# Kernel tuning notes

Hardware: AMD Instinct MI355X
Metric: run time of the kernel (lower is better)

Reference implementation:

```python
import jax, jax.numpy as jnp
import numpy as np

DISCOUNT = 0.997
LAMBDA = 0.95
LOSS_SCALE = 0.5
NUM_BINS = 255
BIN_LO, BIN_HI = -20.0, 20.0


def setup_inputs() -> dict:
    key = jax.random.key(0)
    k0, k1, k2, k3 = jax.random.split(key, 4)
    B, H, D = 1024, 16, 4096
    latents = jax.random.normal(k0, (B, H, D), dtype=jnp.float32)
    rewards = jax.random.normal(k1, (B, H), dtype=jnp.float32)
    dones = jnp.zeros((B, H), dtype=jnp.float32)
    bootstrap_latent = jax.random.normal(k2, (B, D), dtype=jnp.float32)
    W = jax.random.normal(k3, (D, NUM_BINS), dtype=jnp.float32) * (1.0 / np.sqrt(D))
    b = jnp.zeros((NUM_BINS,), dtype=jnp.float32)
    return {"latents": latents, "rewards": rewards, "dones": dones,
            "bootstrap_latent": bootstrap_latent, "W": W, "b": b}


def _bin_centers():
    return jnp.linspace(BIN_LO, BIN_HI, NUM_BINS, dtype=jnp.float32)


def _value_head(x, W, b):
    # x: (N, D) -> logits (N, K), value (N,)
    logits = x @ W + b
    value = jax.nn.softmax(logits, axis=-1) @ _bin_centers()
    return value, logits


def _target_to_bins(returns_flat):
    # two-hot encoding onto uniform bins; returns (N, K) soft target
    step = (BIN_HI - BIN_LO) / (NUM_BINS - 1)
    pos = (jnp.clip(returns_flat, BIN_LO, BIN_HI) - BIN_LO) / step  # in [0, K-1]
    low = jnp.clip(jnp.floor(pos).astype(jnp.int32), 0, NUM_BINS - 2)
    frac = pos - low.astype(pos.dtype)
    oh_lo = jax.nn.one_hot(low, NUM_BINS, dtype=returns_flat.dtype)
    oh_hi = jax.nn.one_hot(low + 1, NUM_BINS, dtype=returns_flat.dtype)
    return (1.0 - frac)[:, None] * oh_lo + frac[:, None] * oh_hi


def _lambda_returns(rewards, values, dones, bootstrap_value):
    # backward linear recurrence: G_t = r_t + gamma*mask_t*((1-lam)*V_{t+1} + lam*G_{t+1})
    next_values = jnp.concatenate([values[:, 1:], bootstrap_value[:, None]], axis=1)
    xs = (rewards.T, next_values.T, (1.0 - dones).T)  # time-major (H, B)

    def step(carry, x):
        r, nv, m = x
        g = r + DISCOUNT * m * ((1.0 - LAMBDA) * nv + LAMBDA * carry)
        return g, g

    _, outs = jax.lax.scan(step, bootstrap_value, xs, reverse=True)
    return outs.T  # (B, H)


def reference(latents, rewards, dones, bootstrap_latent, W, b):
    B, H = rewards.shape
    flat_latents = latents.reshape(-1, latents.shape[-1])  # (B*H, D)
    values_flat, logits = _value_head(flat_latents, W, b)
    values = values_flat.reshape(B, H)

    bootstrap_value, _ = _value_head(bootstrap_latent, W, b)
    bootstrap_value = jax.lax.stop_gradient(bootstrap_value)

    returns = jax.lax.stop_gradient(
        _lambda_returns(rewards, jax.lax.stop_gradient(values), dones, bootstrap_value))

    target = _target_to_bins(returns.reshape(-1))  # (B*H, K)
    logp = jax.nn.log_softmax(logits, axis=-1)
    value_loss = jnp.mean(-jnp.sum(target * logp, axis=-1))
    total_loss = LOSS_SCALE * value_loss

    return jnp.stack([total_loss, value_loss, values.mean(), returns.mean(),
                      jnp.std(values, ddof=1), jnp.std(returns, ddof=1)])
```

## Files before the change

### kernel.cpp

```cpp
#include <hip/hip_runtime.h>
#include <math.h>

#define NBINS 255
#define BIN_LO_F (-20.0f)
#define BIN_HI_F (20.0f)

typedef __attribute__((ext_vector_type(8))) short short8;
typedef __attribute__((ext_vector_type(16))) float f32x16;

__device__ __forceinline__ unsigned short f2bf(float f) {
    unsigned u = __builtin_bit_cast(unsigned, f);
    unsigned r = u + 0x7fffu + ((u >> 16) & 1u);
    return (unsigned short)(r >> 16);
}

__device__ __forceinline__ unsigned pkbf(float lo, float hi) {
    unsigned d;
    asm("v_cvt_pk_bf16_f32 %0, %1, %2" : "=v"(d) : "v"(lo), "v"(hi));
    return d;
}

__device__ __forceinline__ short8 mk8(unsigned a, unsigned b, unsigned c, unsigned d) {
    union { unsigned u[4]; short8 s; } t;
    t.u[0] = a; t.u[1] = b; t.u[2] = c; t.u[3] = d;
    return t.s;
}

__device__ __forceinline__ void glds16(const void* g, void* l) {
    __builtin_amdgcn_global_load_lds(
        (const __attribute__((address_space(1))) unsigned int*)g,
        (__attribute__((address_space(3))) unsigned int*)l, 16, 0, 0);
}

__device__ __forceinline__ double wave_reduce_sum_d(double v) {
    #pragma unroll
    for (int m = 32; m >= 1; m >>= 1) v += __shfl_xor(v, m, 64);
    return v;
}

__global__ __launch_bounds__(256) void pack_w5(
    const float* __restrict__ W, char* __restrict__ WpackB)
{
    int u = blockIdx.x * 256 + threadIdx.x;
    int kt = u >> 9;
    int v  = u & 511;
    int lh = v >> 8;
    int gcol = (v >> 5) & 7;
    int c31  = v & 31;
    int col  = gcol * 32 + c31;
    int k0   = kt * 16 + lh * 8;
    short8 s;
    #pragma unroll
    for (int e = 0; e < 8; ++e)
        s[e] = (col < NBINS) ? (short)f2bf(W[(size_t)(k0 + e) * NBINS + col]) : (short)0;
    *(short8*)(WpackB + (size_t)u * 16) = s;
}

__global__ __launch_bounds__(256, 4) void gemm_mfma_v10(
    const float* __restrict__ latents, const float* __restrict__ boot,
    const char* __restrict__ WpackB, float* __restrict__ P0, float* __restrict__ P1,
    int NR, int R, int D, int nMt)
{
    __shared__ __align__(16) char ldsA[2][4096];
    __shared__ __align__(16) char ldsB[2][8192];

    const int tid  = threadIdx.x;
    const int wave = tid >> 6, lane = tid & 63;
    const int l31  = lane & 31, lhi = lane >> 5;
    const int mw   = wave & 1, nw = wave >> 1;
    const int KH   = D >> 1;
    const int NT   = KH >> 4;

    int bid  = blockIdx.x;
    int work = (bid & 7) * 68 + (bid >> 3);
    const int kh = (work >= nMt) ? 1 : 0;
    const int mt = work - kh * nMt;
    const int row0 = mt * 64;
    float* __restrict__ P = kh ? P1 : P0;

    int arow = row0 + lane; if (arow > R - 1) arow = R - 1;
    const float* arowp = (arow < NR) ? latents + (size_t)arow * D
                                     : boot + (size_t)(arow - NR) * D;
    const float* asrc = arowp + kh * KH + wave * 4;
    const char*  bbase = WpackB + (size_t)kh * ((size_t)NT * 8192)
                                + (wave << 11) + (lane << 4);

    f32x16 acc[4];
    #pragma unroll
    for (int g = 0; g < 4; ++g)
        #pragma unroll
        for (int r = 0; r < 16; ++r) acc[g][r] = 0.f;

#define STAGE(T, BUF) do {                                                  \
        glds16(asrc + (size_t)(T) * 16, &ldsA[BUF][(wave << 10) + (lane << 4)]); \
        const char* bs_ = bbase + (size_t)(T) * 8192;                       \
        char* bd_ = &ldsB[BUF][(wave << 11) + (lane << 4)];                 \
        glds16(bs_,        bd_);                                            \
        glds16(bs_ + 1024, bd_ + 1024);                                     \
    } while (0)

#define COMPUTE(BUF) do {                                                   \
        const char* ab_ = &ldsA[BUF][0] + (lhi << 11) + (mw << 9) + (l31 << 4); \
        const char* bb_ = &ldsB[BUF][0] + (lhi << 12) + (nw << 11) + (l31 << 4); \
        float4 f0_ = *(const float4*)(ab_);                                 \
        float4 f1_ = *(const float4*)(ab_ + 1024);                          \
        short8 a_ = mk8(pkbf(f0_.x, f0_.y), pkbf(f0_.z, f0_.w),             \
                        pkbf(f1_.x, f1_.y), pkbf(f1_.z, f1_.w));            \
        _Pragma("unroll")                                                   \
        for (int g = 0; g < 4; ++g) {                                       \
            short8 b_ = *(const short8*)(bb_ + (g << 9));                   \
            acc[g] = __builtin_amdgcn_mfma_f32_32x32x16_bf16(a_, b_, acc[g], 0, 0, 0); \
        }                                                                   \
    } while (0)

#define BAR()   __builtin_amdgcn_s_barrier()
#define SCHED() __builtin_amdgcn_sched_barrier(0)
#define WAITV3() asm volatile("s_waitcnt vmcnt(3)" ::: "memory")
#define WAITV0() asm volatile("s_waitcnt vmcnt(0)" ::: "memory")

    STAGE(0, 0);

    int t = 0;
    for (; t + 3 < NT; t += 2) {
        BAR(); SCHED(); STAGE(t + 1, 1); SCHED(); WAITV3(); BAR(); SCHED(); COMPUTE(0);
        BAR(); SCHED(); STAGE(t + 2, 0); SCHED(); WAITV3(); BAR(); SCHED(); COMPUTE(1);
    }
    BAR(); SCHED(); STAGE(NT - 1, 1); SCHED(); WAITV3(); BAR(); SCHED(); COMPUTE(0);
    BAR(); SCHED(); WAITV0(); BAR(); SCHED(); COMPUTE(1);

#undef STAGE
#undef COMPUTE
#undef BAR
#undef SCHED
#undef WAITV3
#undef WAITV0

    #pragma unroll
    for (int g = 0; g < 4; ++g) {
        int col = nw * 128 + g * 32 + l31;
        #pragma unroll
        for (int r = 0; r < 16; ++r) {
            int row = row0 + mw * 32 + (r & 3) + 8 * (r >> 2) + 4 * lhi;
            P[(size_t)row * 256 + col] = acc[g][r];
        }
    }
}

__global__ __launch_bounds__(256) void softmax_stats2(
    const float* __restrict__ P0, const float* __restrict__ P1,
    const float* __restrict__ bvec, float* __restrict__ values,
    float* __restrict__ logZ, int R)
{
    int row  = blockIdx.x * 4 + (threadIdx.x >> 6);
    int lane = threadIdx.x & 63;
    if (row >= R) return;
    const float* p0 = P0 + (size_t)row * 256;
    const float* p1 = P1 + (size_t)row * 256;
    const float step = (float)(40.0 / 254.0);

    float l[4];
    float m = -INFINITY;
    #pragma unroll
    for (int u = 0; u < 4; ++u) {
        int idx = lane + 64 * u;
        l[u] = (idx < NBINS) ? (p0[idx] + p1[idx] + bvec[idx]) : -INFINITY;
        m = fmaxf(m, l[u]);
    }
    #pragma unroll
    for (int sh = 32; sh >= 1; sh >>= 1) m = fmaxf(m, __shfl_xor(m, sh, 64));

    float s = 0.f, sc = 0.f;
    #pragma unroll
    for (int u = 0; u < 4; ++u) {
        int idx = lane + 64 * u;
        if (idx < NBINS) {
            float e = __expf(l[u] - m);
            s  += e;
            sc += e * (BIN_LO_F + step * (float)idx);
        }
    }
    #pragma unroll
    for (int sh = 32; sh >= 1; sh >>= 1) {
        s  += __shfl_xor(s, sh, 64);
        sc += __shfl_xor(sc, sh, 64);
    }
    if (lane == 0) {
        values[row] = sc / s;
        logZ[row]   = m + __logf(s);
    }
}

__global__ void lambda_returns_k(
    const float* __restrict__ rewards, const float* __restrict__ dones,
    const float* __restrict__ values, float* __restrict__ returns,
    int B, int H, int NR)
{
    int b = blockIdx.x * blockDim.x + threadIdx.x;
    if (b >= B) return;
    const float gamma = 0.997f;
    const float lam   = 0.95f;
    const float oml   = (float)(1.0 - 0.95);
    float bootv = values[NR + b];
    float g = bootv;
    for (int h = H - 1; h >= 0; --h) {
        float nv   = (h == H - 1) ? bootv : values[b * H + h + 1];
        float mask = 1.0f - dones[b * H + h];
        g = rewards[b * H + h] + gamma * mask * (oml * nv + lam * g);
        returns[b * H + h] = g;
    }
}

__global__ __launch_bounds__(256) void loss_moments2(
    const float* __restrict__ P0, const float* __restrict__ P1,
    const float* __restrict__ bvec, const float* __restrict__ logZ,
    const float* __restrict__ values, const float* __restrict__ returns,
    double* __restrict__ accum, int NR)
{
    int row = blockIdx.x * blockDim.x + threadIdx.x;
    double lsum = 0, vsum = 0, v2 = 0, rsum = 0, r2 = 0;
    if (row < NR) {
        float v   = values[row];
        float ret = returns[row];
        float cl  = fminf(fmaxf(ret, BIN_LO_F), BIN_HI_F);
        const float step = (float)(40.0 / 254.0);
        float pos = (cl - BIN_LO_F) / step;
        int low = (int)floorf(pos);
        low = min(max(low, 0), NBINS - 2);
        float frac = pos - (float)low;
        size_t base = (size_t)row * 256;
        float llo = P0[base + low]     + P1[base + low]     + bvec[low];
        float lhi = P0[base + low + 1] + P1[base + low + 1] + bvec[low + 1];
        float loss = logZ[row] - (1.f - frac) * llo - frac * lhi;
        lsum = (double)loss;
        vsum = (double)v;   v2 = (double)v * (double)v;
        rsum = (double)ret; r2 = (double)ret * (double)ret;
    }
    lsum = wave_reduce_sum_d(lsum);
    vsum = wave_reduce_sum_d(vsum);
    v2   = wave_reduce_sum_d(v2);
    rsum = wave_reduce_sum_d(rsum);
    r2   = wave_reduce_sum_d(r2);
    if ((threadIdx.x & 63) == 0) {
        atomicAdd(&accum[0], lsum);
        atomicAdd(&accum[1], vsum);
        atomicAdd(&accum[2], v2);
        atomicAdd(&accum[3], rsum);
        atomicAdd(&accum[4], r2);
    }
}

__global__ void finalize_k(const double* __restrict__ accum,
                           float* __restrict__ out, int NR)
{
    if (threadIdx.x == 0 && blockIdx.x == 0) {
        double n  = (double)NR;
        double vl = accum[0] / n;
        double mv = accum[1] / n;
        double vv = (accum[2] - n * mv * mv) / (n - 1.0);
        double mr = accum[3] / n;
        double vr = (accum[4] - n * mr * mr) / (n - 1.0);
        out[0] = (float)(0.5 * vl);
        out[1] = (float)vl;
        out[2] = (float)mv;
        out[3] = (float)mr;
        out[4] = (float)sqrt(vv > 0.0 ? vv : 0.0);
        out[5] = (float)sqrt(vr > 0.0 ? vr : 0.0);
    }
}

extern "C" void kernel_launch(void* const* d_in, const int* in_sizes, int n_in,
                              void* d_out, int out_size, void* d_ws, size_t ws_size,
                              hipStream_t stream) {
    const float* latents = (const float*)d_in[0];
    const float* rewards = (const float*)d_in[1];
    const float* dones   = (const float*)d_in[2];
    const float* boot    = (const float*)d_in[3];
    const float* W       = (const float*)d_in[4];
    const float* bvec    = (const float*)d_in[5];
    float* out = (float*)d_out;

    const int BH = in_sizes[1];
    const int D  = in_sizes[0] / BH;
    const int B  = in_sizes[3] / D;
    const int H  = BH / B;
    const int NR = BH;
    const int R  = NR + B;

    char* ws = (char*)d_ws;
    size_t off = 0;
    float* P0 = (float*)(ws + off); off += (size_t)R * 256 * sizeof(float);
    float* P1 = (float*)(ws + off); off += (size_t)R * 256 * sizeof(float);
    float* values = (float*)(ws + off); off += (size_t)R * sizeof(float);
    float* logZ   = (float*)(ws + off); off += (size_t)R * sizeof(float);
    float* rets   = (float*)(ws + off); off += (size_t)NR * sizeof(float);
    off = (off + 255) & ~(size_t)255;
    double* accum = (double*)(ws + off); off += 64;
    off = (off + 255) & ~(size_t)255;
    char* WpackB  = ws + off; off += (size_t)(D / 16) * 8192;

    hipMemsetAsync(accum, 0, 64, stream);

    const int packUnits = (D / 16) * 512;
    pack_w5<<<packUnits / 256, 256, 0, stream>>>(W, WpackB);

    const int nMt = R / 64;
    const int nwg = nMt * 2;
    gemm_mfma_v10<<<nwg, 256, 0, stream>>>(latents, boot, WpackB, P0, P1,
                                           NR, R, D, nMt);
    softmax_stats2<<<(R + 3) / 4, 256, 0, stream>>>(P0, P1, bvec, values, logZ, R);
    lambda_returns_k<<<(B + 255) / 256, 256, 0, stream>>>(rewards, dones, values, rets, B, H, NR);
    loss_moments2<<<(NR + 255) / 256, 256, 0, stream>>>(P0, P1, bvec, logZ, values, rets, accum, NR);
    finalize_k<<<1, 64, 0, stream>>>(accum, out, NR);
}
```

Before: 191.0 us.

## Generalize split-K to four partials and swizzle A-tile LDS layout

Generalizes the GEMM's K split from a fixed two halves to a runtime split (four when the workspace is large enough), so the grid launches twice as many workgroups over R/64 row tiles. It also changes how A rows are loaded into LDS, with an XOR swizzle on 16-byte chunks, to cut bank conflicts on the float4 reads. The softmax and loss kernels now sum the split partials in a loop. In exchange it writes and rereads twice as many partial logit buffers, which adds memory traffic, and it depends on ws_size being large enough.

```diff
diff --git a/kernel.cpp b/kernel.cpp
--- a/kernel.cpp
+++ b/kernel.cpp
@@ -56,10 +56,10 @@
     *(short8*)(WpackB + (size_t)u * 16) = s;
 }
 
-__global__ __launch_bounds__(256, 4) void gemm_mfma_v10(
+__global__ __launch_bounds__(256, 4) void gemm_mfma_v11(
     const float* __restrict__ latents, const float* __restrict__ boot,
-    const char* __restrict__ WpackB, float* __restrict__ P0, float* __restrict__ P1,
-    int NR, int R, int D, int nMt)
+    const char* __restrict__ WpackB, float* __restrict__ P, size_t Pstride,
+    int NR, int R, int D, int split, int nMt, int nwg8)
 {
     __shared__ __align__(16) char ldsA[2][4096];
     __shared__ __align__(16) char ldsB[2][8192];
@@ -68,28 +68,35 @@
     const int wave = tid >> 6, lane = tid & 63;
     const int l31  = lane & 31, lhi = lane >> 5;
     const int mw   = wave & 1, nw = wave >> 1;
-    const int KH   = D >> 1;
-    const int NT   = KH >> 4;
+    const int KQ   = D / split;
+    const int NT   = KQ >> 4;
 
     int bid  = blockIdx.x;
-    int work = (bid & 7) * 68 + (bid >> 3);
-    const int kh = (work >= nMt) ? 1 : 0;
-    const int mt = work - kh * nMt;
+    int work = (bid & 7) * nwg8 + (bid >> 3);
+    const int kq = work / nMt;
+    const int mt = work - kq * nMt;
     const int row0 = mt * 64;
-    float* __restrict__ P = kh ? P1 : P0;
-
-    int arow = row0 + lane; if (arow > R - 1) arow = R - 1;
+    float* __restrict__ Pq = P + (size_t)kq * Pstride;
+
+    const int rloc = (wave << 4) + (lane >> 2);
+    int arow = row0 + rloc; if (arow > R - 1) arow = R - 1;
     const float* arowp = (arow < NR) ? latents + (size_t)arow * D
                                      : boot + (size_t)(arow - NR) * D;
-    const float* asrc = arowp + kh * KH + wave * 4;
-    const char*  bbase = WpackB + (size_t)kh * ((size_t)NT * 8192)
-                                + (wave << 11) + (lane << 4);
+    const float* asrc = arowp + kq * KQ + (((lane & 3) ^ ((rloc >> 1) & 3)) << 2);
+
+    const char* bbase = WpackB + (size_t)kq * ((size_t)NT * 8192)
+                               + (wave << 11) + (lane << 4);
 
     f32x16 acc[4];
     #pragma unroll
     for (int g = 0; g < 4; ++g)
         #pragma unroll
         for (int r = 0; r < 16; ++r) acc[g][r] = 0.f;
+
+    const int ar   = mw * 32 + l31;
+    const int aswz = (ar >> 1) & 3;
+    const int aoff0 = ar * 64 + (((2 * lhi)     ^ aswz) << 4);
+    const int aoff1 = ar * 64 + ((((2 * lhi) | 1) ^ aswz) << 4);
 
 #define STAGE(T, BUF) do {                                                  \
         glds16(asrc + (size_t)(T) * 16, &ldsA[BUF][(wave << 10) + (lane << 4)]); \
@@ -100,10 +107,10 @@
     } while (0)
 
 #define COMPUTE(BUF) do {                                                   \
-        const char* ab_ = &ldsA[BUF][0] + (lhi << 11) + (mw << 9) + (l31 << 4); \
+        const char* ab_ = &ldsA[BUF][0];                                    \
         const char* bb_ = &ldsB[BUF][0] + (lhi << 12) + (nw << 11) + (l31 << 4); \
-        float4 f0_ = *(const float4*)(ab_);                                 \
-        float4 f1_ = *(const float4*)(ab_ + 1024);                          \
+        float4 f0_ = *(const float4*)(ab_ + aoff0);                         \
+        float4 f1_ = *(const float4*)(ab_ + aoff1);                         \
         short8 a_ = mk8(pkbf(f0_.x, f0_.y), pkbf(f0_.z, f0_.w),             \
                         pkbf(f1_.x, f1_.y), pkbf(f1_.z, f1_.w));            \
         _Pragma("unroll")                                                   \
@@ -141,21 +148,20 @@
         #pragma unroll
         for (int r = 0; r < 16; ++r) {
             int row = row0 + mw * 32 + (r & 3) + 8 * (r >> 2) + 4 * lhi;
-            P[(size_t)row * 256 + col] = acc[g][r];
+            Pq[(size_t)row * 256 + col] = acc[g][r];
         }
     }
 }
 
-__global__ __launch_bounds__(256) void softmax_stats2(
-    const float* __restrict__ P0, const float* __restrict__ P1,
+__global__ __launch_bounds__(256) void softmax_statsN(
+    const float* __restrict__ P, size_t Pstride, int split,
     const float* __restrict__ bvec, float* __restrict__ values,
     float* __restrict__ logZ, int R)
 {
     int row  = blockIdx.x * 4 + (threadIdx.x >> 6);
     int lane = threadIdx.x & 63;
     if (row >= R) return;
-    const float* p0 = P0 + (size_t)row * 256;
-    const float* p1 = P1 + (size_t)row * 256;
+    const float* pr = P + (size_t)row * 256;
     const float step = (float)(40.0 / 254.0);
 
     float l[4];
@@ -163,7 +169,11 @@
     #pragma unroll
     for (int u = 0; u < 4; ++u) {
         int idx = lane + 64 * u;
-        l[u] = (idx < NBINS) ? (p0[idx] + p1[idx] + bvec[idx]) : -INFINITY;
+        if (idx < NBINS) {
+            float s = bvec[idx];
+            for (int q = 0; q < split; ++q) s += pr[(size_t)q * Pstride + idx];
+            l[u] = s;
+        } else l[u] = -INFINITY;
         m = fmaxf(m, l[u]);
     }
     #pragma unroll
@@ -210,8 +220,8 @@
     }
 }
 
-__global__ __launch_bounds__(256) void loss_moments2(
-    const float* __restrict__ P0, const float* __restrict__ P1,
+__global__ __launch_bounds__(256) void loss_momentsN(
+    const float* __restrict__ P, size_t Pstride, int split,
     const float* __restrict__ bvec, const float* __restrict__ logZ,
     const float* __restrict__ values, const float* __restrict__ returns,
     double* __restrict__ accum, int NR)
@@ -228,8 +238,11 @@
         low = min(max(low, 0), NBINS - 2);
         float frac = pos - (float)low;
         size_t base = (size_t)row * 256;
-        float llo = P0[base + low]     + P1[base + low]     + bvec[low];
-        float lhi = P0[base + low + 1] + P1[base + low + 1] + bvec[low + 1];
+        float llo = bvec[low], lhi = bvec[low + 1];
+        for (int q = 0; q < split; ++q) {
+            llo += P[(size_t)q * Pstride + base + low];
+            lhi += P[(size_t)q * Pstride + base + low + 1];
+        }
         float loss = logZ[row] - (1.f - frac) * llo - frac * lhi;
         lsum = (double)loss;
         vsum = (double)v;   v2 = (double)v * (double)v;
@@ -286,10 +299,14 @@
     const int NR = BH;
     const int R  = NR + B;
 
+    const size_t Pstride = (size_t)R * 256;
+    const size_t fixed   = (size_t)R * 2 * 4 + (size_t)NR * 4 + 512 +
+                           (size_t)(D / 16) * 8192 + 4096;
+    int split = (ws_size >= 4 * Pstride * 4 + fixed) ? 4 : 2;
+
     char* ws = (char*)d_ws;
     size_t off = 0;
-    float* P0 = (float*)(ws + off); off += (size_t)R * 256 * sizeof(float);
-    float* P1 = (float*)(ws + off); off += (size_t)R * 256 * sizeof(float);
+    float* P = (float*)(ws + off); off += (size_t)split * Pstride * sizeof(float);
     float* values = (float*)(ws + off); off += (size_t)R * sizeof(float);
     float* logZ   = (float*)(ws + off); off += (size_t)R * sizeof(float);
     float* rets   = (float*)(ws + off); off += (size_t)NR * sizeof(float);
@@ -304,11 +321,13 @@
     pack_w5<<<packUnits / 256, 256, 0, stream>>>(W, WpackB);
 
     const int nMt = R / 64;
-    const int nwg = nMt * 2;
-    gemm_mfma_v10<<<nwg, 256, 0, stream>>>(latents, boot, WpackB, P0, P1,
-                                           NR, R, D, nMt);
-    softmax_stats2<<<(R + 3) / 4, 256, 0, stream>>>(P0, P1, bvec, values, logZ, R);
+    const int nwg = nMt * split;
+    gemm_mfma_v11<<<nwg, 256, 0, stream>>>(latents, boot, WpackB, P, Pstride,
+                                           NR, R, D, split, nMt, nwg / 8);
+    softmax_statsN<<<(R + 3) / 4, 256, 0, stream>>>(P, Pstride, split, bvec,
+                                                    values, logZ, R);
     lambda_returns_k<<<(B + 255) / 256, 256, 0, stream>>>(rewards, dones, values, rets, B, H, NR);
-    loss_moments2<<<(NR + 255) / 256, 256, 0, stream>>>(P0, P1, bvec, logZ, values, rets, accum, NR);
+    loss_momentsN<<<(NR + 255) / 256, 256, 0, stream>>>(P, Pstride, split, bvec, logZ,
+                                                        values, rets, accum, NR);
     finalize_k<<<1, 64, 0, stream>>>(accum, out, NR);
 }
```

Measured after the change: 185.6 us. 2.8% less time.
